# Optimization experiments

Hardware: AMD Instinct MI355X
Metric: run time of the kernel (lower is better)

## Reference

```python
import jax, jax.numpy as jnp
import numpy as np

B, N, C, H, R = 64, 197, 768, 12, 98   # batch, tokens, dim, heads, eliminated tokens
SPARSITY, ALPHA = 0.2, 0.1
EPS = 1e-5  # torch nn.LayerNorm default


def layernorm(x, g, b):
    m = jnp.mean(x, axis=-1, keepdims=True)
    v = jnp.var(x, axis=-1, keepdims=True)
    return (x - m) / jnp.sqrt(v + EPS) * g + b


def setup_inputs() -> dict:
    key = jax.random.key(0)
    ks = jax.random.split(key, 8)
    s = lambda k, sh: (jax.random.normal(k, sh, jnp.float32) * 0.02)
    return dict(
        x=jax.random.normal(ks[0], (B, N, C), jnp.float32),
        norm1_g=jnp.ones((C,), jnp.float32), norm1_b=jnp.zeros((C,), jnp.float32),
        qkv_w=s(ks[1], (C, 3 * C)),                      # qkv_bias=False
        proj_w=s(ks[2], (C, C)), proj_b=jnp.zeros((C,), jnp.float32),
        norm2_g=jnp.ones((C,), jnp.float32), norm2_b=jnp.zeros((C,), jnp.float32),
        fc1_w=s(ks[3], (C, 4 * C)), fc1_b=jnp.zeros((4 * C,), jnp.float32),
        fc2_w=s(ks[4], (4 * C, C)), fc2_b=jnp.zeros((C,), jnp.float32),
    )


def reference(x, norm1_g, norm1_b, qkv_w, proj_w, proj_b,
              norm2_g, norm2_b, fc1_w, fc1_b, fc2_w, fc2_b):
    Dh = C // H
    scale = Dh ** -0.5
    # --- attention block ---
    h = layernorm(x, norm1_g, norm1_b)
    qkv = (h @ qkv_w).reshape(B, N, 3, H, Dh).transpose(2, 0, 3, 1, 4)
    q, k, v = qkv[0] * scale, qkv[1], qkv[2]
    attn = jax.nn.softmax(jnp.einsum('bhnd,bhmd->bhnm', q, k), axis=-1)  # [B,H,N,N]
    out = jnp.einsum('bhnm,bhmd->bhnd', attn, v).transpose(0, 2, 1, 3).reshape(B, N, C)
    x = x + out @ proj_w + proj_b
    # --- selection: DiagAttn (head-mean attention diagonal, excluding CLS) ---
    diag = jnp.diagonal(attn.mean(1), axis1=1, axis2=2)[:, 1:]          # [B, N-1]
    token_rank = jnp.argsort(-diag, axis=1) + 1                          # indices into [1, N)
    nk = N - 1 - R                                                       # kept image tokens
    idx_kept = jnp.sort(jnp.concatenate(
        [jnp.zeros((B, 1), token_rank.dtype), token_rank[:, :nk]], axis=1), axis=1)  # [B, K]
    idx_elim = jnp.sort(token_rank[:, nk:], axis=1)                      # [B, R]
    K = nk + 1
    # --- propagate: ThresholdGraph (multihead=True, threshold=True) ---
    x_kept = jnp.take_along_axis(x, idx_kept[:, :, None], axis=1)        # [B, K, C]
    x_elim = jnp.take_along_axis(x, idx_elim[:, :, None], axis=1)        # [B, R, C]
    w = jnp.take_along_axis(attn, idx_kept[:, None, :, None], axis=2)    # [B,H,K,N]
    w = jnp.take_along_axis(w, idx_elim[:, None, None, :], axis=3)       # [B,H,K,R]
    thr_idx = int(R * K * SPARSITY)
    w_sorted = -jnp.sort(-w.reshape(B, H, K * R), axis=-1)               # descending
    thr = w_sorted[:, :, thr_idx][:, :, None, None]
    w = jnp.where(w >= thr, w, jnp.zeros((), w.dtype))
    x_prop = jnp.einsum('bhke,behd->bkhd', w, x_elim.reshape(B, R, H, Dh)).reshape(B, K, C)
    x = x_kept + ALPHA * x_prop                                          # [B, K, C]
    # --- mlp block ---
    h2 = layernorm(x, norm2_g, norm2_b)
    h2 = jax.nn.gelu(h2 @ fc1_w + fc1_b, approximate=False) @ fc2_w + fc2_b
    return x + h2
```

## Files before the change

kernel.cpp:

```cpp
#include <hip/hip_runtime.h>
#include <math.h>

#define NTOK 197
#define CD   768
#define NH   12
#define DH   64
#define NBATCH 64
#define RTOK 98
#define KTOK 99
#define THRN 1941
#define WTOT (KTOK*RTOK)

typedef __attribute__((ext_vector_type(8))) short short8;
typedef __attribute__((ext_vector_type(8))) unsigned short u16x8;
typedef __attribute__((ext_vector_type(4))) float floatx4;

__device__ __forceinline__ int clamp196(int v){ return ((unsigned)v > 196u) ? 196 : v; }
__device__ __forceinline__ unsigned short f2b(float f){
  unsigned u = __float_as_uint(f);
  return (unsigned short)((u + 0x7FFFu + ((u>>16)&1u)) >> 16);
}
__device__ __forceinline__ float us2f(unsigned short u){ return __uint_as_float(((unsigned)u)<<16); }
__device__ __forceinline__ int swz(int row, int q){ return q ^ (((row>>1)&3)<<3); }

__global__ __launch_bounds__(256) void fill_kernel(float* __restrict__ out, int n, float val)
{
  int i = blockIdx.x*256 + threadIdx.x;
  if (i < n) out[i] = val;
}

__global__ __launch_bounds__(256) void tcast_k(const float* __restrict__ src, int K, int ldn, int col0,
                                               unsigned short* __restrict__ dst)
{
  __shared__ float t[32][33];
  int n0 = blockIdx.x*32, k0 = blockIdx.y*32;
  int lx = threadIdx.x & 31, ly = threadIdx.x >> 5;
#pragma unroll
  for (int i=0;i<4;i++)
    t[ly + i*8][lx] = src[(long)(k0 + ly + i*8)*ldn + col0 + n0 + lx];
  __syncthreads();
#pragma unroll
  for (int i=0;i<4;i++){
    int n = ly + i*8;
    dst[(long)(n0 + n)*K + k0 + lx] = f2b(t[lx][n]);
  }
}

__global__ __launch_bounds__(256) void tcast3_k(const float* __restrict__ src, int K, int ldn, int col0,
                                                unsigned short* __restrict__ dsth,
                                                unsigned short* __restrict__ dstl)
{
  __shared__ float t[32][33];
  int n0 = blockIdx.x*32, k0 = blockIdx.y*32;
  int lx = threadIdx.x & 31, ly = threadIdx.x >> 5;
#pragma unroll
  for (int i=0;i<4;i++)
    t[ly + i*8][lx] = src[(long)(k0 + ly + i*8)*ldn + col0 + n0 + lx];
  __syncthreads();
#pragma unroll
  for (int i=0;i<4;i++){
    int n = ly + i*8;
    float v = t[lx][n];
    unsigned short h = f2b(v);
    dsth[(long)(n0 + n)*K + k0 + lx] = h;
    dstl[(long)(n0 + n)*K + k0 + lx] = f2b(v - us2f(h));
  }
}

__global__ __launch_bounds__(256) void ln_kernel(const float* __restrict__ xin,
                                                 const float* __restrict__ gam,
                                                 const float* __restrict__ bet,
                                                 unsigned short* __restrict__ outh,
                                                 unsigned short* __restrict__ outl)
{
  int row = blockIdx.x;
  int tid = threadIdx.x;
  long base = (long)row * CD;
  float v[3];
#pragma unroll
  for (int i=0;i<3;i++) v[i] = xin[base + tid + i*256];
  float s  = v[0]+v[1]+v[2];
  float s2 = v[0]*v[0]+v[1]*v[1]+v[2]*v[2];
#pragma unroll
  for (int off=32; off; off>>=1){ s += __shfl_down(s,off); s2 += __shfl_down(s2,off); }
  __shared__ float ps[4], ps2[4], mb[2];
  if ((tid&63)==0){ ps[tid>>6]=s; ps2[tid>>6]=s2; }
  __syncthreads();
  if (tid==0){
    float S  = ps[0]+ps[1]+ps[2]+ps[3];
    float S2 = ps2[0]+ps2[1]+ps2[2]+ps2[3];
    float m  = S / (float)CD;
    float var = S2 / (float)CD - m*m;
    mb[0]=m; mb[1]=1.0f/sqrtf(var + 1e-5f);
  }
  __syncthreads();
  float m=mb[0], inv=mb[1];
#pragma unroll
  for (int i=0;i<3;i++){
    int c = tid + i*256;
    float r = (v[i]-m)*inv*gam[c] + bet[c];
    unsigned short h = f2b(r);
    outh[base+c] = h;
    if (outl) outl[base+c] = f2b(r - us2f(h));
  }
}

struct GemmP {
  const float* A;
  const void*  B;
  void*        C;
  int M, N, K, ldb, ldc;
  int zdiv;
  long as0, as1, bs0, bs1, cs0, cs1;
};

template<int EPI, int BF16B>
__global__ __launch_bounds__(256) void gemm_k(GemmP p)
{
  __shared__ float As[16][64];
  __shared__ float Bs[16][64];
  int z = blockIdx.z;
  int zq = z / p.zdiv, zr = z - zq*p.zdiv;
  long aoff = zq*p.as0 + zr*p.as1;
  long boff = zq*p.bs0 + zr*p.bs1;
  long coff = zq*p.cs0 + zr*p.cs1;
  int m0 = blockIdx.y*64, n0 = blockIdx.x*64;
  int tid = threadIdx.x;
  int tx = tid & 15, ty = tid >> 4;
  int am = tid >> 2, ak = (tid & 3) * 4;
  int bk = tid >> 4, bn = (tid & 15) * 4;
  bool aVec = ((p.K & 3) == 0);
  float acc[4][4] = {};
  for (int k0 = 0; k0 < p.K; k0 += 16) {
    float aa[4] = {0.f,0.f,0.f,0.f};
    {
      int gm = m0 + am;
      if (gm < p.M) {
        const float* ap = p.A + aoff + (long)gm*p.K + k0 + ak;
        if (aVec) {
          float4 t = *(const float4*)ap;
          aa[0]=t.x; aa[1]=t.y; aa[2]=t.z; aa[3]=t.w;
        } else {
#pragma unroll
          for (int i=0;i<4;i++) if (k0+ak+i < p.K) aa[i] = ap[i];
        }
      }
    }
    float bb[4] = {0.f,0.f,0.f,0.f};
    {
      int gk = k0 + bk;
      if (gk < p.K) {
        long idx = boff + (long)gk*p.ldb + n0 + bn;
        if (BF16B) {
          const unsigned short* bp = (const unsigned short*)p.B + idx;
          if (n0 + bn + 3 < p.N) {
            ushort4 t = *(const ushort4*)bp;
            bb[0]=us2f(t.x); bb[1]=us2f(t.y); bb[2]=us2f(t.z); bb[3]=us2f(t.w);
          } else {
#pragma unroll
            for (int i=0;i<4;i++) if (n0+bn+i < p.N) bb[i] = us2f(bp[i]);
          }
        } else {
          const float* bp = (const float*)p.B + idx;
          if (n0 + bn + 3 < p.N) {
            float4 t = *(const float4*)bp;
            bb[0]=t.x; bb[1]=t.y; bb[2]=t.z; bb[3]=t.w;
          } else {
#pragma unroll
            for (int i=0;i<4;i++) if (n0+bn+i < p.N) bb[i] = bp[i];
          }
        }
      }
    }
    __syncthreads();
#pragma unroll
    for (int i=0;i<4;i++) As[ak+i][am] = aa[i];
#pragma unroll
    for (int i=0;i<4;i++) Bs[bk][bn+i] = bb[i];
    __syncthreads();
#pragma unroll
    for (int kk=0;kk<16;kk++){
      float4 av = *(const float4*)&As[kk][ty*4];
      float4 bv = *(const float4*)&Bs[kk][tx*4];
      float av4[4]={av.x,av.y,av.z,av.w};
      float bv4[4]={bv.x,bv.y,bv.z,bv.w};
#pragma unroll
      for (int i=0;i<4;i++)
#pragma unroll
        for (int j=0;j<4;j++) acc[i][j] = fmaf(av4[i], bv4[j], acc[i][j]);
    }
  }
#pragma unroll
  for (int i=0;i<4;i++){
    int gm = m0 + ty*4 + i;
    if (gm >= p.M) continue;
#pragma unroll
    for (int j=0;j<4;j++){
      int gn = n0 + tx*4 + j;
      if (gn >= p.N) continue;
      float val = acc[i][j];
      if (EPI == 2) {
        ((unsigned short*)p.C)[coff + (long)gm*p.ldc + gn] = f2b(val);
      } else {
        ((float*)p.C)[coff + (long)gm*p.ldc + gn] = val;
      }
    }
  }
}

struct MmP {
  const unsigned short* A;
  const unsigned short* B;
  void* C;
  const float* bias;
  const float* resid;
  unsigned short* vout;
  int M, N, K, ldc;
};

template<int EPI>
__global__ __launch_bounds__(256) void mgemm_k(MmP p)
{
  __shared__ short As[128*32];
  __shared__ short Bs[128*32];
  int tid = threadIdx.x;
  int m0 = blockIdx.y*128, n0 = blockIdx.x*128;
  int w = tid>>6, l = tid&63;
  int wm = (w&1)*64, wn = (w>>1)*64;
  int lr = l&15, kq = (l>>4)*8;
  floatx4 acc[4][4];
#pragma unroll
  for (int i=0;i<4;i++)
#pragma unroll
    for (int j=0;j<4;j++) acc[i][j] = (floatx4){0.f,0.f,0.f,0.f};
  int r0i = tid>>2, q0 = (tid&3)*8;
  int r1i = r0i + 64;
  int w0s = swz(r0i, q0), w1s = swz(r1i, q0);
  for (int k0 = 0; k0 < p.K; k0 += 32) {
    u16x8 a0 = {0,0,0,0,0,0,0,0}, a1 = {0,0,0,0,0,0,0,0};
    { int gm = m0 + r0i;
      if (gm < p.M) a0 = *(const u16x8*)(p.A + (long)gm*p.K + k0 + q0); }
    { int gm = m0 + r1i;
      if (gm < p.M) a1 = *(const u16x8*)(p.A + (long)gm*p.K + k0 + q0); }
    u16x8 b0 = *(const u16x8*)(p.B + (long)(n0 + r0i)*p.K + k0 + q0);
    u16x8 b1 = *(const u16x8*)(p.B + (long)(n0 + r1i)*p.K + k0 + q0);
    __syncthreads();
    *(u16x8*)&As[r0i*32 + w0s] = a0;
    *(u16x8*)&As[r1i*32 + w1s] = a1;
    *(u16x8*)&Bs[r0i*32 + w0s] = b0;
    *(u16x8*)&Bs[r1i*32 + w1s] = b1;
    __syncthreads();
    short8 af[4], bfr[4];
#pragma unroll
    for (int mt=0;mt<4;mt++){ int rr = wm + mt*16 + lr; af[mt]  = *(short8*)&As[rr*32 + swz(rr,kq)]; }
#pragma unroll
    for (int nt=0;nt<4;nt++){ int rr = wn + nt*16 + lr; bfr[nt] = *(short8*)&Bs[rr*32 + swz(rr,kq)]; }
#pragma unroll
    for (int mt=0;mt<4;mt++)
#pragma unroll
      for (int nt=0;nt<4;nt++)
        acc[mt][nt] = __builtin_amdgcn_mfma_f32_16x16x32_bf16(af[mt], bfr[nt], acc[mt][nt], 0, 0, 0);
  }
  int rbase = (l>>4)*4;
#pragma unroll
  for (int mt=0;mt<4;mt++){
#pragma unroll
    for (int r=0;r<4;r++){
      int gm = m0 + wm + mt*16 + rbase + r;
      if (gm >= p.M) continue;
#pragma unroll
      for (int nt=0;nt<4;nt++){
        int gn = n0 + wn + nt*16 + lr;
        float val = acc[mt][nt][r];
        if (EPI == 1) {
          int cb = gm / NTOK, tok = gm - cb*NTOK;
          int h = gn >> 6, d = gn & 63;
          p.vout[(((long)cb*NH + h)*NTOK + tok)*DH + d] = f2b(val);
        } else if (EPI == 2) {
          ((float*)p.C)[(long)gm*p.ldc + gn] = val + p.bias[gn] + p.resid[(long)gm*p.ldc + gn];
        } else {
          float u = val + p.bias[gn];
          ((unsigned short*)p.C)[(long)gm*p.ldc + gn] = f2b(0.5f*u*(1.0f + erff(u*0.70710678118654752f)));
        }
      }
    }
  }
}

struct Mm3P {
  const unsigned short *Ah, *Al, *Bh, *Bl;
  float* C;
  unsigned short *qh, *ql, *kh, *kl;
  long az, bz, cz;
  int M, N, K, ldc;
};

template<int EPI>
__global__ __launch_bounds__(256) void mgemm3_k(Mm3P p)
{
  __shared__ short Ahs[128*32], Als[128*32], Bhs[128*32], Bls[128*32];
  int tid = threadIdx.x;
  int z = blockIdx.z;
  const unsigned short* Azh = p.Ah + (long)z*p.az;
  const unsigned short* Azl = p.Al + (long)z*p.az;
  const unsigned short* Bzh = p.Bh + (long)z*p.bz;
  const unsigned short* Bzl = p.Bl + (long)z*p.bz;
  int m0 = blockIdx.y*128, n0 = blockIdx.x*128;
  int w = tid>>6, l = tid&63;
  int wm = (w&1)*64, wn = (w>>1)*64;
  int lr = l&15, kq = (l>>4)*8;
  floatx4 acc[4][4];
#pragma unroll
  for (int i=0;i<4;i++)
#pragma unroll
    for (int j=0;j<4;j++) acc[i][j] = (floatx4){0.f,0.f,0.f,0.f};
  int r0i = tid>>2, q0 = (tid&3)*8;
  int r1i = r0i + 64;
  int w0s = swz(r0i, q0), w1s = swz(r1i, q0);
  for (int k0 = 0; k0 < p.K; k0 += 32) {
    u16x8 ah0={0,0,0,0,0,0,0,0}, al0={0,0,0,0,0,0,0,0};
    u16x8 ah1={0,0,0,0,0,0,0,0}, al1={0,0,0,0,0,0,0,0};
    u16x8 bh0={0,0,0,0,0,0,0,0}, bl0={0,0,0,0,0,0,0,0};
    u16x8 bh1={0,0,0,0,0,0,0,0}, bl1={0,0,0,0,0,0,0,0};
    { int gm = m0 + r0i;
      if (gm < p.M) {
        long o = (long)gm*p.K + k0 + q0;
        ah0 = *(const u16x8*)(Azh + o);
        al0 = *(const u16x8*)(Azl + o);
      } }
    { int gm = m0 + r1i;
      if (gm < p.M) {
        long o = (long)gm*p.K + k0 + q0;
        ah1 = *(const u16x8*)(Azh + o);
        al1 = *(const u16x8*)(Azl + o);
      } }
    { int gn = n0 + r0i;
      if (gn < p.N) {
        long o = (long)gn*p.K + k0 + q0;
        bh0 = *(const u16x8*)(Bzh + o);
        bl0 = *(const u16x8*)(Bzl + o);
      } }
    { int gn = n0 + r1i;
      if (gn < p.N) {
        long o = (long)gn*p.K + k0 + q0;
        bh1 = *(const u16x8*)(Bzh + o);
        bl1 = *(const u16x8*)(Bzl + o);
      } }
    __syncthreads();
    *(u16x8*)&Ahs[r0i*32 + w0s] = ah0;
    *(u16x8*)&Ahs[r1i*32 + w1s] = ah1;
    *(u16x8*)&Als[r0i*32 + w0s] = al0;
    *(u16x8*)&Als[r1i*32 + w1s] = al1;
    *(u16x8*)&Bhs[r0i*32 + w0s] = bh0;
    *(u16x8*)&Bhs[r1i*32 + w1s] = bh1;
    *(u16x8*)&Bls[r0i*32 + w0s] = bl0;
    *(u16x8*)&Bls[r1i*32 + w1s] = bl1;
    __syncthreads();
    short8 afh[4], afl[4], bfh[4], bfl[4];
#pragma unroll
    for (int mt=0;mt<4;mt++){
      int rr = wm + mt*16 + lr; int rs = rr*32 + swz(rr,kq);
      afh[mt] = *(short8*)&Ahs[rs];
      afl[mt] = *(short8*)&Als[rs];
    }
#pragma unroll
    for (int nt=0;nt<4;nt++){
      int rr = wn + nt*16 + lr; int rs = rr*32 + swz(rr,kq);
      bfh[nt] = *(short8*)&Bhs[rs];
      bfl[nt] = *(short8*)&Bls[rs];
    }
#pragma unroll
    for (int mt=0;mt<4;mt++)
#pragma unroll
      for (int nt=0;nt<4;nt++){
        acc[mt][nt] = __builtin_amdgcn_mfma_f32_16x16x32_bf16(afh[mt], bfh[nt], acc[mt][nt], 0, 0, 0);
        acc[mt][nt] = __builtin_amdgcn_mfma_f32_16x16x32_bf16(afh[mt], bfl[nt], acc[mt][nt], 0, 0, 0);
        acc[mt][nt] = __builtin_amdgcn_mfma_f32_16x16x32_bf16(afl[mt], bfh[nt], acc[mt][nt], 0, 0, 0);
      }
  }
  int rbase = (l>>4)*4;
#pragma unroll
  for (int mt=0;mt<4;mt++){
#pragma unroll
    for (int r=0;r<4;r++){
      int gm = m0 + wm + mt*16 + rbase + r;
      if (gm >= p.M) continue;
#pragma unroll
      for (int nt=0;nt<4;nt++){
        int gn = n0 + wn + nt*16 + lr;
        if (gn >= p.N) continue;
        float val = acc[mt][nt][r];
        if (EPI == 0) {
          p.C[(long)z*p.cz + (long)gm*p.ldc + gn] = val;
        } else {
          int which = (gn >= CD) ? 1 : 0;
          int rc = gn - which*CD;
          int hd = rc >> 6, dd = rc & 63;
          int cb = gm / NTOK, tok = gm - cb*NTOK;
          long off = (((long)cb*NH + hd)*NTOK + tok)*DH + dd;
          float v = which ? val : val*0.125f;
          unsigned short h = f2b(v);
          unsigned short lo16 = f2b(v - us2f(h));
          if (which) { p.kh[off] = h; p.kl[off] = lo16; }
          else       { p.qh[off] = h; p.ql[off] = lo16; }
        }
      }
    }
  }
}

__global__ __launch_bounds__(256) void softmax_kernel(float* __restrict__ attn)
{
  long row = (long)blockIdx.x*4 + (threadIdx.x>>6);
  int ln = threadIdx.x & 63;
  float* rp = attn + row*NTOK;
  float v[4]; float mx = -3.4e38f;
#pragma unroll
  for (int i=0;i<4;i++){
    int c = ln + i*64;
    v[i] = (c < NTOK) ? rp[c] : -3.4e38f;
    mx = fmaxf(mx, v[i]);
  }
#pragma unroll
  for (int off=32; off; off>>=1) mx = fmaxf(mx, __shfl_xor(mx, off));
  float sum = 0.f;
#pragma unroll
  for (int i=0;i<4;i++){
    int c = ln + i*64;
    v[i] = (c < NTOK) ? expf(v[i]-mx) : 0.f;
    sum += v[i];
  }
#pragma unroll
  for (int off=32; off; off>>=1) sum += __shfl_xor(sum, off);
#pragma unroll
  for (int i=0;i<4;i++){
    int c = ln + i*64;
    if (c < NTOK) rp[c] = v[i] / sum;
  }
}

__global__ __launch_bounds__(256) void select_kernel(const float* __restrict__ attn,
                                                     int* __restrict__ idx_kept,
                                                     int* __restrict__ idx_elim, int b0)
{
  int cb = blockIdx.x, tid = threadIdx.x;
  int b = b0 + cb;
  __shared__ float diag[NTOK-1];
  __shared__ int kept[NTOK];
  if (tid < NTOK-1) {
    int t = tid + 1;
    float s = 0.f;
#pragma unroll
    for (int h=0; h<NH; h++)
      s += attn[(((long)cb*NH + h)*NTOK + t)*NTOK + t];
    diag[tid] = s / 12.0f;
  }
  if (tid < KTOK) idx_kept[b*KTOK + tid] = 0;
  if (tid < RTOK) idx_elim[b*RTOK + tid] = 1;
  __syncthreads();
  if (tid < NTOK-1) {
    float dv = diag[tid];
    int r = 0;
    for (int m=0; m<NTOK-1; m++){
      float dm = diag[m];
      r += ((dm > dv) || (dm == dv && m < tid)) ? 1 : 0;
    }
    kept[tid+1] = (r < (NTOK-1-RTOK)) ? 1 : 0;
  }
  __syncthreads();
  if (tid < NTOK-1) {
    int t = tid + 1;
    if (kept[t]) {
      int pos = 1;
      for (int s2=1; s2<t; s2++) pos += kept[s2];
      if (pos >= 1 && pos < KTOK) idx_kept[b*KTOK + pos] = t;
    } else {
      int pos = 0;
      for (int s2=1; s2<t; s2++) pos += 1 - kept[s2];
      if (pos >= 0 && pos < RTOK) idx_elim[b*RTOK + pos] = t;
    }
  }
  if (tid == 0) idx_kept[b*KTOK] = 0;
}

#define PNEL 38
__global__ __launch_bounds__(256) void prop_kernel(const float* __restrict__ attn,
                                                   const float* __restrict__ x1c,
                                                   const int* __restrict__ idx_kept,
                                                   const int* __restrict__ idx_elim,
                                                   float* __restrict__ x2, int b0)
{
  int z = blockIdx.x;
  int cb = z / NH, h = z - cb*NH;
  int b = b0 + cb;
  int tid = threadIdx.x;
  int wid = tid >> 6, l = tid & 63;
  int lr = l & 15, hi2 = l >> 4;
  __shared__ short WhL[112*128];
  __shared__ short XtL[64*128];
  __shared__ unsigned hist[64];
  __shared__ int kidx[KTOK], eidx[RTOK];
  if (tid < KTOK) kidx[tid] = clamp196(idx_kept[b*KTOK + tid]);
  if (tid < RTOK) eidx[tid] = clamp196(idx_elim[b*RTOK + tid]);
  u16x8 zz = {0,0,0,0,0,0,0,0};
#pragma unroll
  for (int i=0;i<7;i++) *(u16x8*)&WhL[tid*8 + i*2048] = zz;
#pragma unroll
  for (int i=0;i<4;i++) *(u16x8*)&XtL[tid*8 + i*2048] = zz;
  __syncthreads();
  for (int i = tid; i < RTOK*DH; i += 256){
    int e = i >> 6, d = i & 63;
    float v = x1c[((long)cb*NTOK + eidx[e])*CD + h*DH + d];
    XtL[d*128 + (((e>>3) ^ (d&7))<<3) + (e&7)] = (short)f2b(v);
  }
  const float* ab = attn + (long)z*NTOK*NTOK;
  unsigned wb[PNEL];
#pragma unroll
  for (int j=0;j<PNEL;j++){
    int i = tid + (j<<8);
    if (i < WTOT){
      int k = i / RTOK, e = i - k*RTOK;
      wb[j] = __float_as_uint(ab[kidx[k]*NTOK + eidx[e]]);
    } else wb[j] = 0u;
  }
  unsigned P = 0; int rrank = THRN;
  for (int pass=0; pass<5; ++pass){
    int sh = 24 - 6*pass;
    if (tid < 64) hist[tid] = 0u;
    __syncthreads();
#pragma unroll
    for (int j=0;j<PNEL;j++){
      int i = tid + (j<<8);
      unsigned v = wb[j];
      bool m = (i < WTOT) && ((pass == 0) || ((v >> (sh+6)) == P));
      if (m) atomicAdd(&hist[(v>>sh)&63u], 1u);
    }
    __syncthreads();
    unsigned cum = 0; int bsel = 0; unsigned above = 0;
    for (int bb=63; bb>=0; --bb){
      unsigned hv = hist[bb];
      if (cum + hv >= (unsigned)rrank){ bsel = bb; above = cum; break; }
      cum += hv;
    }
    P = (P<<6) | (unsigned)bsel;
    rrank -= (int)above;
    __syncthreads();
  }
  unsigned thrbits = P;
#pragma unroll
  for (int j=0;j<PNEL;j++){
    int i = tid + (j<<8);
    if (i < WTOT){
      int k = i / RTOK, e = i - k*RTOK;
      unsigned v = (wb[j] >= thrbits) ? wb[j] : 0u;
      WhL[k*128 + (((e>>3) ^ (k&7))<<3) + (e&7)] = (short)f2b(__uint_as_float(v));
    }
  }
  __syncthreads();
  floatx4 acc[7];
#pragma unroll
  for (int mt=0;mt<7;mt++) acc[mt] = (floatx4){0.f,0.f,0.f,0.f};
  short8 bfr[4];
#pragma unroll
  for (int ks=0;ks<4;ks++){
    int c = ks*4 + hi2;
    int rd = wid*16 + lr;
    bfr[ks] = *(short8*)&XtL[rd*128 + ((c ^ (lr&7))<<3)];
  }
#pragma unroll
  for (int mt=0;mt<7;mt++){
#pragma unroll
    for (int ks=0;ks<4;ks++){
      int c = ks*4 + hi2;
      int rw = mt*16 + lr;
      short8 af = *(short8*)&WhL[rw*128 + ((c ^ (lr&7))<<3)];
      acc[mt] = __builtin_amdgcn_mfma_f32_16x16x32_bf16(af, bfr[ks], acc[mt], 0, 0, 0);
    }
  }
#pragma unroll
  for (int mt=0;mt<7;mt++){
#pragma unroll
    for (int r=0;r<4;r++){
      int kt = mt*16 + hi2*4 + r;
      if (kt >= KTOK) continue;
      int d = wid*16 + lr;
      float xk = x1c[((long)cb*NTOK + kidx[kt])*CD + h*DH + d];
      x2[((long)b*KTOK + kt)*CD + h*DH + d] = xk + 0.1f*acc[mt][r];
    }
  }
}

extern "C" void kernel_launch(void* const* d_in, const int* in_sizes, int n_in,
                              void* d_out, int out_size, void* d_ws, size_t ws_size,
                              hipStream_t stream)
{
  const float* x     = (const float*)d_in[0];
  const float* n1g   = (const float*)d_in[1];
  const float* n1b   = (const float*)d_in[2];
  const float* qkvw  = (const float*)d_in[3];
  const float* projw = (const float*)d_in[4];
  const float* projb = (const float*)d_in[5];
  const float* n2g   = (const float*)d_in[6];
  const float* n2b   = (const float*)d_in[7];
  const float* fc1w  = (const float*)d_in[8];
  const float* fc1b  = (const float*)d_in[9];
  const float* fc2w  = (const float*)d_in[10];
  const float* fc2b  = (const float*)d_in[11];
  float* out = (float*)d_out;

  const long XROW = (long)NTOK*CD;
  const long AH   = (long)NTOK*NTOK;
  const long AB   = (long)NH*AH;
  const long QH   = (long)NH*NTOK*DH;
  const long SMALL = 6336L + 6272L;
  const long WFIX  = 1769472L;
  const long PB = AB + 3*XROW + XROW/2;
  const long MLPFIX = 2359296L;
  const long MINREQ = SMALL + WFIX + (MLPFIX + 64*1920L > PB ? MLPFIX + 64*1920L : PB);

  long wsf = (long)(ws_size / 4);
  if (wsf < MINREQ) {
    float val = (float)(ws_size >> 20) * 1000.0f + 1.0f;
    fill_kernel<<<dim3((out_size+255)/256), 256, 0, stream>>>(out, out_size, val);
    return;
  }

  long avail = wsf - SMALL - WFIX;
  int G = (int)(avail / PB);
  if (G > NBATCH) G = NBATCH;
  if (G < 1) G = 1;
  long rcl = ((avail - MLPFIX) / 1920L) / 64L * 64L;
  int RC = (int)(rcl > 6336L ? 6336L : rcl);
  if (RC < 64) RC = 64;

  float* ws = (float*)d_ws;
  int*   idx_kept = (int*)ws;
  int*   idx_elim = idx_kept + 6336;
  unsigned short* qkwh   = (unsigned short*)(ws + SMALL);
  unsigned short* qkwl   = qkwh + 1179648;
  unsigned short* qkvwvT = qkwl + 1179648;
  unsigned short* projwT = qkvwvT + 589824;
  float* base  = ws + SMALL + WFIX;
  float* attnc = base;
  unsigned short* qh = (unsigned short*)(base + (long)G*AB);
  unsigned short* ql = qh + (long)G*XROW;
  float* x1c = (float*)qh;
  unsigned short* kh = (unsigned short*)(base + (long)G*AB + (long)G*XROW);
  unsigned short* kl = kh + (long)G*XROW;
  unsigned short* aoutb = kh;
  unsigned short* vc = (unsigned short*)(base + (long)G*AB + 2L*G*XROW);
  unsigned short* h1h = (unsigned short*)(base + (long)G*AB + 2L*G*XROW + (long)G*XROW/2);
  unsigned short* h1l = h1h + (long)G*XROW;
  unsigned short* fc1wT = (unsigned short*)base;
  unsigned short* fc2wT = fc1wT + 2359296;
  unsigned short* h2b   = (unsigned short*)(base + MLPFIX);
  unsigned short* gb    = h2b + (long)RC*CD;

  tcast3_k<<<dim3(48,24), 256, 0, stream>>>(qkvw, CD, 3*CD, 0, qkwh, qkwl);
  tcast_k <<<dim3(24,24), 256, 0, stream>>>(qkvw, CD, 3*CD, 2*CD, qkvwvT);
  tcast_k <<<dim3(24,24), 256, 0, stream>>>(projw, CD, CD, 0, projwT);

  for (int b0 = 0; b0 < NBATCH; b0 += G) {
    int GL = (NBATCH - b0 < G) ? (NBATCH - b0) : G;
    int MROW = GL*NTOK;
    ln_kernel<<<dim3(MROW), 256, 0, stream>>>(x + (long)b0*XROW, n1g, n1b, h1h, h1l);
    {
      Mm3P p{}; p.Ah=h1h; p.Al=h1l; p.Bh=qkwh; p.Bl=qkwl;
      p.qh=qh; p.ql=ql; p.kh=kh; p.kl=kl;
      p.M=MROW; p.N=2*CD; p.K=CD; p.ldc=0; p.az=0; p.bz=0; p.cz=0;
      mgemm3_k<1><<<dim3(12,(MROW+127)/128,1), 256, 0, stream>>>(p);
    }
    {
      MmP p{}; p.A=h1h; p.B=qkvwvT; p.vout=vc;
      p.M=MROW; p.N=CD; p.K=CD; p.ldc=CD;
      mgemm_k<1><<<dim3(6,(MROW+127)/128,1), 256, 0, stream>>>(p);
    }
    {
      Mm3P p{}; p.Ah=qh; p.Al=ql; p.Bh=kh; p.Bl=kl; p.C=attnc;
      p.M=NTOK; p.N=NTOK; p.K=DH; p.ldc=NTOK;
      p.az=(long)NTOK*DH; p.bz=(long)NTOK*DH; p.cz=AH;
      mgemm3_k<0><<<dim3(2,2,GL*NH), 256, 0, stream>>>(p);
    }
    softmax_kernel<<<dim3(GL*591), 256, 0, stream>>>(attnc);
    select_kernel<<<dim3(GL), 256, 0, stream>>>(attnc, idx_kept, idx_elim, b0);
    {
      GemmP p{}; p.A=attnc; p.B=vc; p.C=aoutb;
      p.M=NTOK; p.N=DH; p.K=NTOK; p.ldb=DH; p.ldc=CD; p.zdiv=NH;
      p.as0=AB; p.as1=AH; p.bs0=QH; p.bs1=(long)NTOK*DH; p.cs0=XROW; p.cs1=DH;
      gemm_k<2,1><<<dim3(1,4,GL*NH), 256, 0, stream>>>(p);
    }
    {
      MmP p{}; p.A=aoutb; p.B=projwT; p.C=x1c;
      p.M=MROW; p.N=CD; p.K=CD; p.ldc=CD;
      p.bias=projb; p.resid=x + (long)b0*XROW;
      mgemm_k<2><<<dim3(6,(MROW+127)/128,1), 256, 0, stream>>>(p);
    }
    prop_kernel<<<dim3(GL*NH), 256, 0, stream>>>(attnc, x1c, idx_kept, idx_elim, out, b0);
  }

  tcast_k<<<dim3(96,24), 256, 0, stream>>>(fc1w, CD, 4*CD, 0, fc1wT);
  tcast_k<<<dim3(24,96), 256, 0, stream>>>(fc2w, 4*CD, CD, 0, fc2wT);

  for (int r0 = 0; r0 < NBATCH*KTOK; r0 += RC) {
    int RCL = (NBATCH*KTOK - r0 < RC) ? (NBATCH*KTOK - r0) : RC;
    ln_kernel<<<dim3(RCL), 256, 0, stream>>>(out + (long)r0*CD, n2g, n2b, h2b, nullptr);
    {
      MmP p{}; p.A=h2b; p.B=fc1wT; p.C=gb;
      p.M=RCL; p.N=4*CD; p.K=CD; p.ldc=4*CD; p.bias=fc1b;
      mgemm_k<3><<<dim3(24,(RCL+127)/128,1), 256, 0, stream>>>(p);
    }
    {
      MmP p{}; p.A=gb; p.B=fc2wT; p.C=out + (long)r0*CD;
      p.M=RCL; p.N=CD; p.K=4*CD; p.ldc=CD;
      p.bias=fc2b; p.resid=out + (long)r0*CD;
      mgemm_k<2><<<dim3(6,(RCL+127)/128,1), 256, 0, stream>>>(p);
    }
  }
}
```

Measured before the change: 775.7 us.

## Move attention-times-V product from FP32 SIMT GEMM to split-bf16 MFMA kernel

Replaces the generic FP32 tiled GEMM for attn@V with a dedicated MFMA kernel. The kernel splits the fp32 attention probabilities into hi/lo bf16 pairs on load to preserve accuracy, and reads V from a new transposed copy produced by an extra vtrans kernel. This is meant to cut the scalar FMA cost of the PV product. In exchange it adds a transpose launch, reuses the h1h buffer for V^T, and doubles the MFMA work for the hi/lo split.

Measured after the change: 763.2 us. Within noise of the previous version (-1.6%).

```diff
diff --git a/kernel.cpp b/kernel.cpp
--- a/kernel.cpp
+++ b/kernel.cpp
@@ -23,6 +23,24 @@
 __device__ __forceinline__ float us2f(unsigned short u){ return __uint_as_float(((unsigned)u)<<16); }
 __device__ __forceinline__ int swz(int row, int q){ return q ^ (((row>>1)&3)<<3); }
 
+__device__ __forceinline__ void ldsplit(const float* ap, int rem, u16x8& h, u16x8& l){
+  float v[8];
+  if (rem >= 8) {
+    float4 t0 = *(const float4*)ap, t1 = *(const float4*)(ap+4);
+    v[0]=t0.x; v[1]=t0.y; v[2]=t0.z; v[3]=t0.w;
+    v[4]=t1.x; v[5]=t1.y; v[6]=t1.z; v[7]=t1.w;
+  } else {
+#pragma unroll
+    for (int j=0;j<8;j++) v[j] = (j < rem) ? ap[j] : 0.f;
+  }
+#pragma unroll
+  for (int j=0;j<8;j++){
+    unsigned short hh = f2b(v[j]);
+    h[j] = hh;
+    l[j] = f2b(v[j] - us2f(hh));
+  }
+}
+
 __global__ __launch_bounds__(256) void fill_kernel(float* __restrict__ out, int n, float val)
 {
   int i = blockIdx.x*256 + threadIdx.x;
@@ -67,6 +85,29 @@
   }
 }
 
+__global__ __launch_bounds__(256) void vtrans_k(const unsigned short* __restrict__ src,
+                                                unsigned short* __restrict__ dst)
+{
+  __shared__ unsigned short t[32][33];
+  int z = blockIdx.z;
+  int t0 = blockIdx.x*32, d0 = blockIdx.y*32;
+  int lx = threadIdx.x & 31, ly = threadIdx.x >> 5;
+  const unsigned short* s = src + (long)z*NTOK*DH;
+  unsigned short* o = dst + (long)z*DH*NTOK;
+#pragma unroll
+  for (int i=0;i<4;i++){
+    int tok = t0 + ly + i*8;
+    t[ly+i*8][lx] = (tok < NTOK) ? s[(long)tok*DH + d0 + lx] : (unsigned short)0;
+  }
+  __syncthreads();
+#pragma unroll
+  for (int i=0;i<4;i++){
+    int d = d0 + ly + i*8;
+    int tok = t0 + lx;
+    if (tok < NTOK) o[(long)d*NTOK + tok] = t[lx][ly+i*8];
+  }
+}
+
 __global__ __launch_bounds__(256) void ln_kernel(const float* __restrict__ xin,
                                                  const float* __restrict__ gam,
                                                  const float* __restrict__ bet,
@@ -105,104 +146,85 @@
   }
 }
 
-struct GemmP {
-  const float* A;
-  const void*  B;
-  void*        C;
-  int M, N, K, ldb, ldc;
-  int zdiv;
-  long as0, as1, bs0, bs1, cs0, cs1;
+struct PvP {
+  const float* P;
+  const unsigned short* Vt;
+  unsigned short* C;
 };
 
-template<int EPI, int BF16B>
-__global__ __launch_bounds__(256) void gemm_k(GemmP p)
-{
-  __shared__ float As[16][64];
-  __shared__ float Bs[16][64];
+__global__ __launch_bounds__(256) void pv_k(PvP p)
+{
+  __shared__ short Ahs[128*32], Als[128*32], Bs[64*32];
+  int tid = threadIdx.x;
   int z = blockIdx.z;
-  int zq = z / p.zdiv, zr = z - zq*p.zdiv;
-  long aoff = zq*p.as0 + zr*p.as1;
-  long boff = zq*p.bs0 + zr*p.bs1;
-  long coff = zq*p.cs0 + zr*p.cs1;
-  int m0 = blockIdx.y*64, n0 = blockIdx.x*64;
-  int tid = threadIdx.x;
-  int tx = tid & 15, ty = tid >> 4;
-  int am = tid >> 2, ak = (tid & 3) * 4;
-  int bk = tid >> 4, bn = (tid & 15) * 4;
-  bool aVec = ((p.K & 3) == 0);
-  float acc[4][4] = {};
-  for (int k0 = 0; k0 < p.K; k0 += 16) {
-    float aa[4] = {0.f,0.f,0.f,0.f};
-    {
-      int gm = m0 + am;
-      if (gm < p.M) {
-        const float* ap = p.A + aoff + (long)gm*p.K + k0 + ak;
-        if (aVec) {
-          float4 t = *(const float4*)ap;
-          aa[0]=t.x; aa[1]=t.y; aa[2]=t.z; aa[3]=t.w;
-        } else {
-#pragma unroll
-          for (int i=0;i<4;i++) if (k0+ak+i < p.K) aa[i] = ap[i];
-        }
+  int cb = z / NH, h = z - cb*NH;
+  const float* Az = p.P + (long)z*NTOK*NTOK;
+  const unsigned short* Bz = p.Vt + (long)z*DH*NTOK;
+  int m0 = blockIdx.y*128;
+  int w = tid>>6, l = tid&63;
+  int wm = (w&1)*64, wn = (w>>1)*32;
+  int lr = l&15, kq = (l>>4)*8;
+  floatx4 acc[4][2];
+#pragma unroll
+  for (int i=0;i<4;i++)
+#pragma unroll
+    for (int j=0;j<2;j++) acc[i][j] = (floatx4){0.f,0.f,0.f,0.f};
+  int r0i = tid>>2, q0 = (tid&3)*8;
+  int r1i = r0i + 64;
+  int w0s = swz(r0i, q0), w1s = swz(r1i, q0);
+  for (int k0 = 0; k0 < NTOK; k0 += 32) {
+    u16x8 ah0={0,0,0,0,0,0,0,0}, al0={0,0,0,0,0,0,0,0};
+    u16x8 ah1={0,0,0,0,0,0,0,0}, al1={0,0,0,0,0,0,0,0};
+    u16x8 b0 ={0,0,0,0,0,0,0,0};
+    int rem = NTOK - k0 - q0;
+    { int gm = m0 + r0i;
+      if (gm < NTOK && rem > 0) ldsplit(Az + (long)gm*NTOK + k0 + q0, rem, ah0, al0); }
+    { int gm = m0 + r1i;
+      if (gm < NTOK && rem > 0) ldsplit(Az + (long)gm*NTOK + k0 + q0, rem, ah1, al1); }
+    { const unsigned short* bp = Bz + (long)r0i*NTOK + k0 + q0;
+      if (rem >= 8) b0 = *(const u16x8*)bp;
+      else if (rem > 0) {
+#pragma unroll
+        for (int j=0;j<8;j++) if (j < rem) b0[j] = bp[j];
+      } }
+    __syncthreads();
+    *(u16x8*)&Ahs[r0i*32 + w0s] = ah0;
+    *(u16x8*)&Ahs[r1i*32 + w1s] = ah1;
+    *(u16x8*)&Als[r0i*32 + w0s] = al0;
+    *(u16x8*)&Als[r1i*32 + w1s] = al1;
+    *(u16x8*)&Bs [r0i*32 + w0s] = b0;
+    __syncthreads();
+    short8 afh[4], afl[4], bfr[2];
+#pragma unroll
+    for (int mt=0;mt<4;mt++){
+      int rr = wm + mt*16 + lr; int rs = rr*32 + swz(rr,kq);
+      afh[mt] = *(short8*)&Ahs[rs];
+      afl[mt] = *(short8*)&Als[rs];
+    }
+#pragma unroll
+    for (int nt=0;nt<2;nt++){
+      int rr = wn + nt*16 + lr;
+      bfr[nt] = *(short8*)&Bs[rr*32 + swz(rr,kq)];
+    }
+#pragma unroll
+    for (int mt=0;mt<4;mt++)
+#pragma unroll
+      for (int nt=0;nt<2;nt++){
+        acc[mt][nt] = __builtin_amdgcn_mfma_f32_16x16x32_bf16(afh[mt], bfr[nt], acc[mt][nt], 0, 0, 0);
+        acc[mt][nt] = __builtin_amdgcn_mfma_f32_16x16x32_bf16(afl[mt], bfr[nt], acc[mt][nt], 0, 0, 0);
       }
-    }
-    float bb[4] = {0.f,0.f,0.f,0.f};
-    {
-      int gk = k0 + bk;
-      if (gk < p.K) {
-        long idx = boff + (long)gk*p.ldb + n0 + bn;
-        if (BF16B) {
-          const unsigned short* bp = (const unsigned short*)p.B + idx;
-          if (n0 + bn + 3 < p.N) {
-            ushort4 t = *(const ushort4*)bp;
-            bb[0]=us2f(t.x); bb[1]=us2f(t.y); bb[2]=us2f(t.z); bb[3]=us2f(t.w);
-          } else {
-#pragma unroll
-            for (int i=0;i<4;i++) if (n0+bn+i < p.N) bb[i] = us2f(bp[i]);
-          }
-        } else {
-          const float* bp = (const float*)p.B + idx;
-          if (n0 + bn + 3 < p.N) {
-            float4 t = *(const float4*)bp;
-            bb[0]=t.x; bb[1]=t.y; bb[2]=t.z; bb[3]=t.w;
-          } else {
-#pragma unroll
-            for (int i=0;i<4;i++) if (n0+bn+i < p.N) bb[i] = bp[i];
-          }
-        }
-      }
-    }
-    __syncthreads();
-#pragma unroll
-    for (int i=0;i<4;i++) As[ak+i][am] = aa[i];
-#pragma unroll
-    for (int i=0;i<4;i++) Bs[bk][bn+i] = bb[i];
-    __syncthreads();
-#pragma unroll
-    for (int kk=0;kk<16;kk++){
-      float4 av = *(const float4*)&As[kk][ty*4];
-      float4 bv = *(const float4*)&Bs[kk][tx*4];
-      float av4[4]={av.x,av.y,av.z,av.w};
-      float bv4[4]={bv.x,bv.y,bv.z,bv.w};
-#pragma unroll
-      for (int i=0;i<4;i++)
-#pragma unroll
-        for (int j=0;j<4;j++) acc[i][j] = fmaf(av4[i], bv4[j], acc[i][j]);
-    }
-  }
-#pragma unroll
-  for (int i=0;i<4;i++){
-    int gm = m0 + ty*4 + i;
-    if (gm >= p.M) continue;
-#pragma unroll
-    for (int j=0;j<4;j++){
-      int gn = n0 + tx*4 + j;
-      if (gn >= p.N) continue;
-      float val = acc[i][j];
-      if (EPI == 2) {
-        ((unsigned short*)p.C)[coff + (long)gm*p.ldc + gn] = f2b(val);
-      } else {
-        ((float*)p.C)[coff + (long)gm*p.ldc + gn] = val;
+  }
+  int rbase = (l>>4)*4;
+#pragma unroll
+  for (int mt=0;mt<4;mt++){
+#pragma unroll
+    for (int r=0;r<4;r++){
+      int gm = m0 + wm + mt*16 + rbase + r;
+      if (gm >= NTOK) continue;
+#pragma unroll
+      for (int nt=0;nt<2;nt++){
+        int gn = wn + nt*16 + lr;
+        p.C[(long)cb*NTOK*CD + (long)gm*CD + h*DH + gn] = f2b(acc[mt][nt][r]);
       }
     }
   }
@@ -611,7 +633,6 @@
   const long XROW = (long)NTOK*CD;
   const long AH   = (long)NTOK*NTOK;
   const long AB   = (long)NH*AH;
-  const long QH   = (long)NH*NTOK*DH;
   const long SMALL = 6336L + 6272L;
   const long WFIX  = 1769472L;
   const long PB = AB + 3*XROW + XROW/2;
@@ -651,6 +672,7 @@
   unsigned short* vc = (unsigned short*)(base + (long)G*AB + 2L*G*XROW);
   unsigned short* h1h = (unsigned short*)(base + (long)G*AB + 2L*G*XROW + (long)G*XROW/2);
   unsigned short* h1l = h1h + (long)G*XROW;
+  unsigned short* vt  = h1h;
   unsigned short* fc1wT = (unsigned short*)base;
   unsigned short* fc2wT = fc1wT + 2359296;
   unsigned short* h2b   = (unsigned short*)(base + MLPFIX);
@@ -675,6 +697,7 @@
       p.M=MROW; p.N=CD; p.K=CD; p.ldc=CD;
       mgemm_k<1><<<dim3(6,(MROW+127)/128,1), 256, 0, stream>>>(p);
     }
+    vtrans_k<<<dim3(7,2,GL*NH), 256, 0, stream>>>(vc, vt);
     {
       Mm3P p{}; p.Ah=qh; p.Al=ql; p.Bh=kh; p.Bl=kl; p.C=attnc;
       p.M=NTOK; p.N=NTOK; p.K=DH; p.ldc=NTOK;
@@ -684,10 +707,8 @@
     softmax_kernel<<<dim3(GL*591), 256, 0, stream>>>(attnc);
     select_kernel<<<dim3(GL), 256, 0, stream>>>(attnc, idx_kept, idx_elim, b0);
     {
-      GemmP p{}; p.A=attnc; p.B=vc; p.C=aoutb;
-      p.M=NTOK; p.N=DH; p.K=NTOK; p.ldb=DH; p.ldc=CD; p.zdiv=NH;
-      p.as0=AB; p.as1=AH; p.bs0=QH; p.bs1=(long)NTOK*DH; p.cs0=XROW; p.cs1=DH;
-      gemm_k<2,1><<<dim3(1,4,GL*NH), 256, 0, stream>>>(p);
+      PvP p{}; p.P=attnc; p.Vt=vt; p.C=aoutb;
+      pv_k<<<dim3(1,2,GL*NH), 256, 0, stream>>>(p);
     }
     {
       MmP p{}; p.A=aoutb; p.B=projwT; p.C=x1c;
```
